# Kernel optimization log

Measured on AMD Instinct MI355X. Metric: run time of the kernel, lower is better.

Reference implementation:

```python
import jax, jax.numpy as jnp
import numpy as np
import math

B, S, HID, H = 1, 512, 256, 8
D = HID // H
SCALE = 1.0 / math.sqrt(D)
PI = math.pi


def setup_inputs() -> dict:
    key = jax.random.key(0)
    ks = jax.random.split(key, 6)
    x = jax.random.normal(ks[0], (B, S, HID), dtype=jnp.float32)
    w = lambda k: jax.random.normal(k, (HID, HID), dtype=jnp.float32) * 0.02
    return {
        'x': x,
        'wq': w(ks[1]), 'bq': jnp.zeros((HID,), jnp.float32),
        'wk': w(ks[2]), 'bk': jnp.zeros((HID,), jnp.float32),
        'wv': w(ks[3]), 'bv': jnp.zeros((HID,), jnp.float32),
        'wo': w(ks[4]), 'bo': jnp.zeros((HID,), jnp.float32),
    }


def _split_heads(t):
    # [B,S,HID] -> [B,H,S,D]
    return t.reshape(B, S, H, D).transpose(0, 2, 1, 3)


def reference(x, wq, bq, wk, bk, wv, bv, wo, bo):
    # Linear projections (torch nn.Linear: x @ W.T + b)
    q = _split_heads(x @ wq.T + bq)
    k = _split_heads(x @ wk.T + bk)
    v = _split_heads(x @ wv.T + bv)

    omega = jax.nn.sigmoid(q) * PI      # [B,H,S,D]
    amplitude = jax.nn.sigmoid(k)       # [B,H,S,D]
    phase = jnp.tanh(v) * PI            # [B,H,S,D]

    # relative position i-j, [S,S]
    pos = (jnp.arange(S)[:, None] - jnp.arange(S)[None, :]).astype(jnp.float32)
    # wave interference tensor [B,H,S,D,S] (query i, dim d, key j)
    interaction = amplitude[..., None] * jnp.cos(
        omega[..., None] * pos[None, None, :, None, :] + phase[..., None])
    patterns = jax.nn.softmax(interaction * SCALE, axis=-1)  # softmax over keys j
    # contract over key positions: per-dim attention
    context = jnp.einsum('bhidj,bhjd->bhid', patterns, v)    # [B,H,S,D]
    context = context.transpose(0, 2, 1, 3).reshape(B, S, HID)
    return context @ wo.T + bo
```

## Files before the change

### kernel.cpp

```cpp
#include <hip/hip_runtime.h>
#include <math.h>

#define SEQ 512
#define HID 256
#define NH 8
#define DH 32
#define PI_F 3.14159265358979323846f
#define SCALE_F 0.17677669529663687f
#define LOG2E_F 1.4426950408889634f

#define OFF_OMEGA 0
#define OFF_AMP   131072
#define OFF_PHASE 262144
#define OFF_V     393216
#define OFF_CTX   524288
#define OFF_PQKV  655360
#define OFF_POUT  2228224

__global__ __launch_bounds__(256) void gemm_slice(
    const float* __restrict__ A,
    const float* __restrict__ W0, const float* __restrict__ W1,
    const float* __restrict__ W2, float* __restrict__ part)
{
    const int which = blockIdx.y;
    const float* W = (which == 0) ? W0 : (which == 1) ? W1 : W2;
    const int bx = blockIdx.x;
    const int ks = bx & 3;
    const int ct = (bx >> 2) & 3;
    const int rt = bx >> 4;
    const int r0 = rt * 64, c0 = ct * 64, k0 = ks * 64;

    __shared__ float xs[64 * 68];
    __shared__ float wts[64 * 64];

    const int tid = threadIdx.x;
#pragma unroll
    for (int it = 0; it < 4; it++) {
        int idx = tid + it * 256;
        int rr = idx >> 4, f4 = idx & 15;
        float4 av = *(const float4*)(A + (r0 + rr) * HID + k0 + 4 * f4);
        *(float4*)&xs[rr * 68 + 4 * f4] = av;
        float4 wv = *(const float4*)(W + (c0 + rr) * HID + k0 + 4 * f4);
        int cw = rr ^ ((f4 & 7) << 2);
        wts[(4 * f4 + 0) * 64 + cw] = wv.x;
        wts[(4 * f4 + 1) * 64 + cw] = wv.y;
        wts[(4 * f4 + 2) * 64 + cw] = wv.z;
        wts[(4 * f4 + 3) * 64 + cw] = wv.w;
    }
    __syncthreads();

    const int rg = tid >> 4, cg = tid & 15;
    float acc[4][4];
#pragma unroll
    for (int i = 0; i < 4; i++)
#pragma unroll
        for (int j = 0; j < 4; j++) acc[i][j] = 0.f;

#pragma unroll
    for (int g = 0; g < 16; g++) {
        float xfa[4][4], wfa[4][4];
#pragma unroll
        for (int i = 0; i < 4; i++) {
            float4 xv = *(const float4*)&xs[(4 * rg + i) * 68 + 4 * g];
            xfa[i][0] = xv.x; xfa[i][1] = xv.y; xfa[i][2] = xv.z; xfa[i][3] = xv.w;
        }
        const int sw = (g & 7) << 2;
#pragma unroll
        for (int m = 0; m < 4; m++) {
            float4 wv = *(const float4*)&wts[(4 * g + m) * 64 + ((4 * cg) ^ sw)];
            wfa[m][0] = wv.x; wfa[m][1] = wv.y; wfa[m][2] = wv.z; wfa[m][3] = wv.w;
        }
#pragma unroll
        for (int m = 0; m < 4; m++)
#pragma unroll
            for (int i = 0; i < 4; i++)
#pragma unroll
                for (int j = 0; j < 4; j++)
                    acc[i][j] = fmaf(xfa[i][m], wfa[m][j], acc[i][j]);
    }

    float* P = part + (size_t)(which * 4 + ks) * (SEQ * HID);
#pragma unroll
    for (int i = 0; i < 4; i++) {
        float4 o;
        o.x = acc[i][0]; o.y = acc[i][1]; o.z = acc[i][2]; o.w = acc[i][3];
        *(float4*)&P[(r0 + 4 * rg + i) * HID + c0 + 4 * cg] = o;
    }
}

__global__ __launch_bounds__(256) void reduce_qkv(
    const float* __restrict__ part,
    const float* __restrict__ bq, const float* __restrict__ bk,
    const float* __restrict__ bv, float* __restrict__ ws)
{
    const int which = blockIdx.y;
    const int r = blockIdx.x, c = threadIdx.x;
    const float* P = part + (size_t)which * 4 * (SEQ * HID) + r * HID + c;
    float s = (P[0] + P[SEQ * HID]) + (P[2 * SEQ * HID] + P[3 * SEQ * HID]);
    const int o = r * HID + c;
    if (which == 0) {
        s += bq[c];
        ws[OFF_OMEGA + o] = PI_F / (1.f + expf(-s));
    } else if (which == 1) {
        s += bk[c];
        ws[OFF_AMP + o] = 1.f / (1.f + expf(-s));
    } else {
        s += bv[c];
        ws[OFF_V + o] = s;
        ws[OFF_PHASE + o] = PI_F * tanhf(s);
    }
}

__global__ __launch_bounds__(256) void reduce_out(
    const float* __restrict__ part, const float* __restrict__ bo,
    float* __restrict__ out)
{
    const int r = blockIdx.x, c = threadIdx.x;
    const float* P = part + r * HID + c;
    float s = (P[0] + P[SEQ * HID]) + (P[2 * SEQ * HID] + P[3 * SEQ * HID]);
    out[r * HID + c] = s + bo[c];
}

__global__ __launch_bounds__(256) void wave_attn(const float* __restrict__ ws,
                                                 float* __restrict__ ctx)
{
    const int h  = blockIdx.y;
    const int il = threadIdx.x >> 5;
    const int d  = threadIdx.x & 31;
    const int i  = blockIdx.x * 8 + il;
    const int col = h * DH + d;

    const float w  = ws[OFF_OMEGA + i * HID + col];
    const float aL = ws[OFF_AMP + i * HID + col] * (SCALE_F * LOG2E_F);
    const float ph = ws[OFF_PHASE + i * HID + col];
    const float* vcol = ws + OFF_V + col;

    float sw_, cw;
    sincosf(w, &sw_, &cw);
    float c2 = cw * cw - sw_ * sw_, s2 = 2.f * sw_ * cw;
    float c4 = c2 * c2 - s2 * s2,   s4 = 2.f * s2 * c2;

    float th0 = fmaf(w, (float)i, ph);
    float s0, cc0;
    sincosf(th0, &s0, &cc0);

    float pc[4], psn[4];
    pc[0] = cc0; psn[0] = s0;
#pragma unroll
    for (int k = 1; k < 4; k++) {
        float nc = pc[k - 1] * cw + psn[k - 1] * sw_;
        float ns = psn[k - 1] * cw - pc[k - 1] * sw_;
        pc[k] = nc; psn[k] = ns;
    }
    float p[4], q[4], den[4], num[4];
#pragma unroll
    for (int k = 0; k < 4; k++) {
        p[k] = aL * pc[k]; q[k] = aL * psn[k];
        den[k] = 0.f; num[k] = 0.f;
    }

#pragma unroll 4
    for (int t = 0; t < SEQ / 4; t++) {
        float v0 = vcol[(4 * t + 0) * HID];
        float v1 = vcol[(4 * t + 1) * HID];
        float v2v = vcol[(4 * t + 2) * HID];
        float v3 = vcol[(4 * t + 3) * HID];
        float e0 = __builtin_amdgcn_exp2f(p[0]);
        float e1 = __builtin_amdgcn_exp2f(p[1]);
        float e2 = __builtin_amdgcn_exp2f(p[2]);
        float e3 = __builtin_amdgcn_exp2f(p[3]);
        den[0] += e0; den[1] += e1; den[2] += e2; den[3] += e3;
        num[0] = fmaf(e0, v0, num[0]);
        num[1] = fmaf(e1, v1, num[1]);
        num[2] = fmaf(e2, v2v, num[2]);
        num[3] = fmaf(e3, v3, num[3]);
#pragma unroll
        for (int k = 0; k < 4; k++) {
            float np = p[k] * c4 + q[k] * s4;
            float nq = q[k] * c4 - p[k] * s4;
            p[k] = np; q[k] = nq;
        }
    }
    float denom = (den[0] + den[1]) + (den[2] + den[3]);
    float numer = (num[0] + num[1]) + (num[2] + num[3]);
    ctx[i * HID + col] = numer / denom;
}

extern "C" void kernel_launch(void* const* d_in, const int* in_sizes, int n_in,
                              void* d_out, int out_size, void* d_ws, size_t ws_size,
                              hipStream_t stream) {
    const float* x  = (const float*)d_in[0];
    const float* wq = (const float*)d_in[1];
    const float* bq = (const float*)d_in[2];
    const float* wk = (const float*)d_in[3];
    const float* bk = (const float*)d_in[4];
    const float* wv = (const float*)d_in[5];
    const float* bv = (const float*)d_in[6];
    const float* wo = (const float*)d_in[7];
    const float* bo = (const float*)d_in[8];

    float* ws = (float*)d_ws;

    hipLaunchKernelGGL(gemm_slice, dim3(128, 3), dim3(256), 0, stream,
                       x, wq, wk, wv, ws + OFF_PQKV);
    hipLaunchKernelGGL(reduce_qkv, dim3(SEQ, 3), dim3(256), 0, stream,
                       ws + OFF_PQKV, bq, bk, bv, ws);
    hipLaunchKernelGGL(wave_attn, dim3(SEQ / 8, NH), dim3(256), 0, stream,
                       ws, ws + OFF_CTX);
    hipLaunchKernelGGL(gemm_slice, dim3(128, 1), dim3(256), 0, stream,
                       ws + OFF_CTX, wo, wo, wo, ws + OFF_POUT);
    hipLaunchKernelGGL(reduce_out, dim3(SEQ), dim3(256), 0, stream,
                       ws + OFF_POUT, bo, (float*)d_out);
}
```

Measured before the change: 107.7 us.

## Fuse split-K GEMM reductions into epilogue and use Chebyshev recurrence in attention

The projection GEMMs drop the split-K partial buffers and separate reduce kernels. Each block now loops over the full K dimension on 32x64 tiles and applies bias plus the sigmoid/tanh activations in its epilogue, which cuts two kernel launches and the partial-sum memory traffic. The wave attention loop replaces the 2D rotation update of (p,q) with a Chebyshev three-term recurrence on the cosine alone, saving FMAs and registers per step. The trade-offs are less GEMM parallelism (64 blocks per matrix instead of 128) and possible extra floating-point drift from the recurrence.

```diff
diff --git a/kernel.cpp b/kernel.cpp
--- a/kernel.cpp
+++ b/kernel.cpp
@@ -14,111 +14,113 @@
 #define OFF_PHASE 262144
 #define OFF_V     393216
 #define OFF_CTX   524288
-#define OFF_PQKV  655360
-#define OFF_POUT  2228224
-
-__global__ __launch_bounds__(256) void gemm_slice(
+
+__device__ __forceinline__ float sigmoidf_(float x) { return 1.f / (1.f + expf(-x)); }
+
+__global__ __launch_bounds__(256) void gemm_fused(
     const float* __restrict__ A,
     const float* __restrict__ W0, const float* __restrict__ W1,
-    const float* __restrict__ W2, float* __restrict__ part)
+    const float* __restrict__ W2,
+    const float* __restrict__ bq, const float* __restrict__ bk,
+    const float* __restrict__ bv, const float* __restrict__ bo,
+    float* __restrict__ ws, float* __restrict__ outp, int mode_base)
 {
-    const int which = blockIdx.y;
-    const float* W = (which == 0) ? W0 : (which == 1) ? W1 : W2;
+    const int mode = mode_base + blockIdx.y;
+    const float* W    = (mode == 1) ? W1 : (mode == 2) ? W2 : W0;
+    const float* bias = (mode == 0) ? bq : (mode == 1) ? bk : (mode == 2) ? bv : bo;
+
     const int bx = blockIdx.x;
-    const int ks = bx & 3;
-    const int ct = (bx >> 2) & 3;
-    const int rt = bx >> 4;
-    const int r0 = rt * 64, c0 = ct * 64, k0 = ks * 64;
-
-    __shared__ float xs[64 * 68];
+    const int ct = bx & 3;
+    const int rt = bx >> 2;
+    const int r0 = rt * 32, c0 = ct * 64;
+
+    __shared__ float xs[32 * 68];
     __shared__ float wts[64 * 64];
 
     const int tid = threadIdx.x;
-#pragma unroll
-    for (int it = 0; it < 4; it++) {
-        int idx = tid + it * 256;
-        int rr = idx >> 4, f4 = idx & 15;
-        float4 av = *(const float4*)(A + (r0 + rr) * HID + k0 + 4 * f4);
-        *(float4*)&xs[rr * 68 + 4 * f4] = av;
-        float4 wv = *(const float4*)(W + (c0 + rr) * HID + k0 + 4 * f4);
-        int cw = rr ^ ((f4 & 7) << 2);
-        wts[(4 * f4 + 0) * 64 + cw] = wv.x;
-        wts[(4 * f4 + 1) * 64 + cw] = wv.y;
-        wts[(4 * f4 + 2) * 64 + cw] = wv.z;
-        wts[(4 * f4 + 3) * 64 + cw] = wv.w;
-    }
-    __syncthreads();
-
     const int rg = tid >> 4, cg = tid & 15;
-    float acc[4][4];
-#pragma unroll
-    for (int i = 0; i < 4; i++)
+
+    float acc[2][4];
+#pragma unroll
+    for (int i = 0; i < 2; i++)
 #pragma unroll
         for (int j = 0; j < 4; j++) acc[i][j] = 0.f;
 
-#pragma unroll
-    for (int g = 0; g < 16; g++) {
-        float xfa[4][4], wfa[4][4];
-#pragma unroll
-        for (int i = 0; i < 4; i++) {
-            float4 xv = *(const float4*)&xs[(4 * rg + i) * 68 + 4 * g];
-            xfa[i][0] = xv.x; xfa[i][1] = xv.y; xfa[i][2] = xv.z; xfa[i][3] = xv.w;
-        }
-        const int sw = (g & 7) << 2;
-#pragma unroll
-        for (int m = 0; m < 4; m++) {
-            float4 wv = *(const float4*)&wts[(4 * g + m) * 64 + ((4 * cg) ^ sw)];
-            wfa[m][0] = wv.x; wfa[m][1] = wv.y; wfa[m][2] = wv.z; wfa[m][3] = wv.w;
-        }
-#pragma unroll
-        for (int m = 0; m < 4; m++)
-#pragma unroll
-            for (int i = 0; i < 4; i++)
-#pragma unroll
-                for (int j = 0; j < 4; j++)
-                    acc[i][j] = fmaf(xfa[i][m], wfa[m][j], acc[i][j]);
-    }
-
-    float* P = part + (size_t)(which * 4 + ks) * (SEQ * HID);
-#pragma unroll
-    for (int i = 0; i < 4; i++) {
-        float4 o;
-        o.x = acc[i][0]; o.y = acc[i][1]; o.z = acc[i][2]; o.w = acc[i][3];
-        *(float4*)&P[(r0 + 4 * rg + i) * HID + c0 + 4 * cg] = o;
-    }
-}
-
-__global__ __launch_bounds__(256) void reduce_qkv(
-    const float* __restrict__ part,
-    const float* __restrict__ bq, const float* __restrict__ bk,
-    const float* __restrict__ bv, float* __restrict__ ws)
-{
-    const int which = blockIdx.y;
-    const int r = blockIdx.x, c = threadIdx.x;
-    const float* P = part + (size_t)which * 4 * (SEQ * HID) + r * HID + c;
-    float s = (P[0] + P[SEQ * HID]) + (P[2 * SEQ * HID] + P[3 * SEQ * HID]);
-    const int o = r * HID + c;
-    if (which == 0) {
-        s += bq[c];
-        ws[OFF_OMEGA + o] = PI_F / (1.f + expf(-s));
-    } else if (which == 1) {
-        s += bk[c];
-        ws[OFF_AMP + o] = 1.f / (1.f + expf(-s));
-    } else {
-        s += bv[c];
-        ws[OFF_V + o] = s;
-        ws[OFF_PHASE + o] = PI_F * tanhf(s);
-    }
-}
-
-__global__ __launch_bounds__(256) void reduce_out(
-    const float* __restrict__ part, const float* __restrict__ bo,
-    float* __restrict__ out)
-{
-    const int r = blockIdx.x, c = threadIdx.x;
-    const float* P = part + r * HID + c;
-    float s = (P[0] + P[SEQ * HID]) + (P[2 * SEQ * HID] + P[3 * SEQ * HID]);
-    out[r * HID + c] = s + bo[c];
+    for (int kc = 0; kc < 4; kc++) {
+        const int k0 = kc * 64;
+#pragma unroll
+        for (int it = 0; it < 4; it++) {
+            int idx = tid + it * 256;
+            int rr = idx >> 4, f4 = idx & 15;
+            float4 wv = *(const float4*)(W + (c0 + rr) * HID + k0 + 4 * f4);
+            int cw = rr ^ ((f4 & 7) << 2);
+            wts[(4 * f4 + 0) * 64 + cw] = wv.x;
+            wts[(4 * f4 + 1) * 64 + cw] = wv.y;
+            wts[(4 * f4 + 2) * 64 + cw] = wv.z;
+            wts[(4 * f4 + 3) * 64 + cw] = wv.w;
+            if (it < 2) {
+                float4 av = *(const float4*)(A + (r0 + rr) * HID + k0 + 4 * f4);
+                *(float4*)&xs[rr * 68 + 4 * f4] = av;
+            }
+        }
+        __syncthreads();
+
+#pragma unroll
+        for (int g = 0; g < 16; g++) {
+            float xfa[2][4], wfa[4][4];
+#pragma unroll
+            for (int i = 0; i < 2; i++) {
+                float4 xv = *(const float4*)&xs[(2 * rg + i) * 68 + 4 * g];
+                xfa[i][0] = xv.x; xfa[i][1] = xv.y; xfa[i][2] = xv.z; xfa[i][3] = xv.w;
+            }
+            const int sw = (g & 7) << 2;
+#pragma unroll
+            for (int m = 0; m < 4; m++) {
+                float4 wv = *(const float4*)&wts[(4 * g + m) * 64 + ((4 * cg) ^ sw)];
+                wfa[m][0] = wv.x; wfa[m][1] = wv.y; wfa[m][2] = wv.z; wfa[m][3] = wv.w;
+            }
+#pragma unroll
+            for (int m = 0; m < 4; m++)
+#pragma unroll
+                for (int i = 0; i < 2; i++)
+#pragma unroll
+                    for (int j = 0; j < 4; j++)
+                        acc[i][j] = fmaf(xfa[i][m], wfa[m][j], acc[i][j]);
+        }
+        __syncthreads();
+    }
+
+    float4 b4 = *(const float4*)&bias[c0 + 4 * cg];
+#pragma unroll
+    for (int i = 0; i < 2; i++) {
+        const int r = r0 + 2 * rg + i;
+        const int o = r * HID + c0 + 4 * cg;
+        float s0 = acc[i][0] + b4.x;
+        float s1 = acc[i][1] + b4.y;
+        float s2 = acc[i][2] + b4.z;
+        float s3 = acc[i][3] + b4.w;
+        if (mode == 0) {
+            float4 t;
+            t.x = PI_F * sigmoidf_(s0); t.y = PI_F * sigmoidf_(s1);
+            t.z = PI_F * sigmoidf_(s2); t.w = PI_F * sigmoidf_(s3);
+            *(float4*)&ws[OFF_OMEGA + o] = t;
+        } else if (mode == 1) {
+            float4 t;
+            t.x = sigmoidf_(s0); t.y = sigmoidf_(s1);
+            t.z = sigmoidf_(s2); t.w = sigmoidf_(s3);
+            *(float4*)&ws[OFF_AMP + o] = t;
+        } else if (mode == 2) {
+            float4 t; t.x = s0; t.y = s1; t.z = s2; t.w = s3;
+            *(float4*)&ws[OFF_V + o] = t;
+            float4 p;
+            p.x = PI_F * tanhf(s0); p.y = PI_F * tanhf(s1);
+            p.z = PI_F * tanhf(s2); p.w = PI_F * tanhf(s3);
+            *(float4*)&ws[OFF_PHASE + o] = p;
+        } else {
+            float4 t; t.x = s0; t.y = s1; t.z = s2; t.w = s3;
+            *(float4*)&outp[o] = t;
+        }
+    }
 }
 
 __global__ __launch_bounds__(256) void wave_attn(const float* __restrict__ ws,
@@ -138,26 +140,32 @@
     float sw_, cw;
     sincosf(w, &sw_, &cw);
     float c2 = cw * cw - sw_ * sw_, s2 = 2.f * sw_ * cw;
-    float c4 = c2 * c2 - s2 * s2,   s4 = 2.f * s2 * c2;
+    float c4 = c2 * c2 - s2 * s2;
 
     float th0 = fmaf(w, (float)i, ph);
-    float s0, cc0;
-    sincosf(th0, &s0, &cc0);
-
-    float pc[4], psn[4];
-    pc[0] = cc0; psn[0] = s0;
-#pragma unroll
-    for (int k = 1; k < 4; k++) {
-        float nc = pc[k - 1] * cw + psn[k - 1] * sw_;
-        float ns = psn[k - 1] * cw - pc[k - 1] * sw_;
-        pc[k] = nc; psn[k] = ns;
-    }
-    float p[4], q[4], den[4], num[4];
+    float c_, s_;
+    sincosf(th0, &s_, &c_);
+
+    float pPrev[4], pCur[4];
 #pragma unroll
     for (int k = 0; k < 4; k++) {
-        p[k] = aL * pc[k]; q[k] = aL * psn[k];
-        den[k] = 0.f; num[k] = 0.f;
-    }
+        pPrev[k] = aL * c_;
+        float nc = c_ * cw + s_ * sw_;
+        float ns = s_ * cw - c_ * sw_;
+        c_ = nc; s_ = ns;
+    }
+#pragma unroll
+    for (int k = 0; k < 4; k++) {
+        pCur[k] = aL * c_;
+        float nc = c_ * cw + s_ * sw_;
+        float ns = s_ * cw - c_ * sw_;
+        c_ = nc; s_ = ns;
+    }
+    const float C2 = 2.f * c4;
+
+    float den[4], num[4];
+#pragma unroll
+    for (int k = 0; k < 4; k++) { den[k] = 0.f; num[k] = 0.f; }
 
 #pragma unroll 4
     for (int t = 0; t < SEQ / 4; t++) {
@@ -165,10 +173,10 @@
         float v1 = vcol[(4 * t + 1) * HID];
         float v2v = vcol[(4 * t + 2) * HID];
         float v3 = vcol[(4 * t + 3) * HID];
-        float e0 = __builtin_amdgcn_exp2f(p[0]);
-        float e1 = __builtin_amdgcn_exp2f(p[1]);
-        float e2 = __builtin_amdgcn_exp2f(p[2]);
-        float e3 = __builtin_amdgcn_exp2f(p[3]);
+        float e0 = __builtin_amdgcn_exp2f(pPrev[0]);
+        float e1 = __builtin_amdgcn_exp2f(pPrev[1]);
+        float e2 = __builtin_amdgcn_exp2f(pPrev[2]);
+        float e3 = __builtin_amdgcn_exp2f(pPrev[3]);
         den[0] += e0; den[1] += e1; den[2] += e2; den[3] += e3;
         num[0] = fmaf(e0, v0, num[0]);
         num[1] = fmaf(e1, v1, num[1]);
@@ -176,9 +184,8 @@
         num[3] = fmaf(e3, v3, num[3]);
 #pragma unroll
         for (int k = 0; k < 4; k++) {
-            float np = p[k] * c4 + q[k] * s4;
-            float nq = q[k] * c4 - p[k] * s4;
-            p[k] = np; q[k] = nq;
+            float nx = fmaf(C2, pCur[k], -pPrev[k]);
+            pPrev[k] = pCur[k]; pCur[k] = nx;
         }
     }
     float denom = (den[0] + den[1]) + (den[2] + den[3]);
@@ -201,14 +208,11 @@
 
     float* ws = (float*)d_ws;
 
-    hipLaunchKernelGGL(gemm_slice, dim3(128, 3), dim3(256), 0, stream,
-                       x, wq, wk, wv, ws + OFF_PQKV);
-    hipLaunchKernelGGL(reduce_qkv, dim3(SEQ, 3), dim3(256), 0, stream,
-                       ws + OFF_PQKV, bq, bk, bv, ws);
+    hipLaunchKernelGGL(gemm_fused, dim3(64, 3), dim3(256), 0, stream,
+                       x, wq, wk, wv, bq, bk, bv, bo, ws, (float*)d_out, 0);
     hipLaunchKernelGGL(wave_attn, dim3(SEQ / 8, NH), dim3(256), 0, stream,
                        ws, ws + OFF_CTX);
-    hipLaunchKernelGGL(gemm_slice, dim3(128, 1), dim3(256), 0, stream,
-                       ws + OFF_CTX, wo, wo, wo, ws + OFF_POUT);
-    hipLaunchKernelGGL(reduce_out, dim3(SEQ), dim3(256), 0, stream,
-                       ws + OFF_POUT, bo, (float*)d_out);
+    hipLaunchKernelGGL(gemm_fused, dim3(64, 1), dim3(256), 0, stream,
+                       ws + OFF_CTX, wo, wo, wo, bq, bk, bv, bo, ws,
+                       (float*)d_out, 3);
 }
```

Measured after the change: 99.95 us. -7.2%, faster.
